# Optimization experiments

Hardware: AMD Instinct MI355X
Metric: run time of the kernel (lower is better)

Reference implementation:

```python
import jax, jax.numpy as jnp
import numpy as np
from jax.scipy.special import logsumexp

C = 1024   # num HMM states
H = 256    # hidden_dim
V = 10000  # vocab size
B = 16     # batch
N = 256    # sequence length
EPS = 1e-5


def _layernorm(x, g, b):
    mu = x.mean(-1, keepdims=True)
    var = ((x - mu) ** 2).mean(-1, keepdims=True)
    return g * (x - mu) * jax.lax.rsqrt(var + EPS) + b


def _residual(x, W1, b1, W2, b2, g, beta):
    # ResidualLayer: ln(relu(lin2(relu(lin1(x)))) + relu(lin1(x))), dropout=0
    h = jax.nn.relu(x @ W1.T + b1)
    return _layernorm(jax.nn.relu(h @ W2.T + b2) + h, g, beta)


def setup_inputs() -> dict:
    key = jax.random.key(0)
    ks = iter(jax.random.split(key, 40))
    def nrm(shape, scale):
        return jax.random.normal(next(ks), shape, dtype=jnp.float32) * scale
    w = 1.0 / np.sqrt(H)
    inp = {}
    # embeddings (torch.randn)
    inp['start_emb'] = nrm((C, H), 1.0)
    inp['state_emb'] = nrm((C, H), 1.0)
    inp['pre_emb'] = nrm((C, H), 1.0)
    # start_mlp: ResidualLayer(H,H) + Linear(H,1)
    for p, out_dim in (('s', 1), ('t', C), ('e', V)):
        inp[p + '_W1'] = nrm((H, H), w)
        inp[p + '_b1'] = jnp.zeros((H,), jnp.float32)
        inp[p + '_W2'] = nrm((H, H), w)
        inp[p + '_b2'] = jnp.zeros((H,), jnp.float32)
        inp[p + '_g'] = jnp.ones((H,), jnp.float32)
        inp[p + '_beta'] = jnp.zeros((H,), jnp.float32)
        inp[p + '_Wo'] = nrm((out_dim, H), w)
        inp[p + '_bo'] = jnp.zeros((out_dim,), jnp.float32)
    inp['text'] = jax.random.randint(next(ks), (B, N), 0, V)
    return inp


def reference(start_emb, state_emb, pre_emb,
              s_W1, s_b1, s_W2, s_b2, s_g, s_beta, s_Wo, s_bo,
              t_W1, t_b1, t_W2, t_b2, t_g, t_beta, t_Wo, t_bo,
              e_W1, e_b1, e_W2, e_b2, e_g, e_beta, e_Wo, e_bo,
              text):
    # start: (C,) log init distribution
    start = jax.nn.log_softmax(
        (_residual(start_emb, s_W1, s_b1, s_W2, s_b2, s_g, s_beta) @ s_Wo.T + s_bo).squeeze(-1))
    # transition[i, j] = log p(z_t = j | z_{t-1} = i), shape (C, C)
    transition = jax.nn.log_softmax(
        _residual(state_emb, t_W1, t_b1, t_W2, t_b2, t_g, t_beta) @ t_Wo.T + t_bo, axis=-1)
    # emission[c, v] = log p(x = v | z = c), shape (C, V)
    emission = jax.nn.log_softmax(
        _residual(pre_emb, e_W1, e_b1, e_W2, e_b2, e_g, e_beta) @ e_Wo.T + e_bo, axis=-1)

    emit = emission.T[text]              # (B, N, C): log p(x_t | z_t = c)
    alpha0 = start[None, :] + emit[:, 0]  # (B, C)

    def step(alpha, e_t):
        # log-semiring matmul: alpha_next[b,j] = lse_i(alpha[b,i] + T[i,j]) + emit
        a = logsumexp(alpha[:, :, None] + transition[None], axis=1) + e_t
        return a, None

    alphaT, _ = jax.lax.scan(step, alpha0, jnp.swapaxes(emit[:, 1:], 0, 1))
    return logsumexp(alphaT, axis=-1).sum()
```

## Files before the change

kernel.cpp:

```cpp
#include <hip/hip_runtime.h>
#include <hip/hip_bf16.h>

typedef __attribute__((ext_vector_type(8))) short short8;
typedef __attribute__((ext_vector_type(4))) float f32x4;
typedef unsigned short ushort;
typedef unsigned long long u64;
typedef unsigned int u32;

#define AL(p) __hip_atomic_load((p), __ATOMIC_RELAXED, __HIP_MEMORY_SCOPE_AGENT)
#define AS(p,v) __hip_atomic_store((p), (v), __ATOMIC_RELAXED, __HIP_MEMORY_SCOPE_AGENT)

__device__ inline ushort f2bf(float x) {
  __hip_bfloat16 h = __float2bfloat16(x);
  return *reinterpret_cast<ushort*>(&h);
}
__device__ inline float bfhi2f(u32 lo) {
  union { u32 u; float f; } c; c.u = lo & 0xFFFF0000u; return c.f;
}
__device__ inline float bflo2f(u32 lo) {
  union { u32 u; float f; } c; c.u = lo << 16; return c.f;
}
__device__ inline u32 pk2(float a, float b) {
  return (u32)f2bf(__expf(a)) | ((u32)f2bf(__expf(b)) << 16);
}

__global__ void cast2_kernel(const float* __restrict__ a, ushort* __restrict__ oa, int na,
                             const float* __restrict__ b, ushort* __restrict__ ob, int nb) {
  int i = blockIdx.x * blockDim.x + threadIdx.x;
  int st = gridDim.x * blockDim.x;
  for (; i < na + nb; i += st) {
    if (i < na) oa[i] = f2bf(a[i]);
    else        ob[i - na] = f2bf(b[i - na]);
  }
}

__global__ __launch_bounds__(256) void mlp3_kernel(
    const float* X0, const float* W10, const float* b10, const float* W20, const float* b20,
    const float* g0, const float* be0, float* of0, ushort* ob0,
    const float* X1, const float* W11, const float* b11, const float* W21, const float* b21,
    const float* g1, const float* be1, float* of1, ushort* ob1,
    const float* X2, const float* W12, const float* b12, const float* W22, const float* b22,
    const float* g2, const float* be2, float* of2, ushort* ob2)
{
  const float *X, *W1, *b1, *W2, *b2, *g, *beta; float* of32; ushort* obf;
  int y = blockIdx.y;
  if (y == 0)      { X=X0; W1=W10; b1=b10; W2=W20; b2=b20; g=g0; beta=be0; of32=of0; obf=ob0; }
  else if (y == 1) { X=X1; W1=W11; b1=b11; W2=W21; b2=b21; g=g1; beta=be1; of32=of1; obf=ob1; }
  else             { X=X2; W1=W12; b1=b12; W2=W22; b2=b22; g=g2; beta=be2; of32=of2; obf=ob2; }

  __shared__ float Xs[16 * 260];
  __shared__ float H1s[16 * 260];
  __shared__ float mu_s[16], rs_s[16];
  int tid = threadIdx.x;
  int r0 = blockIdx.x * 16;
  for (int q = 0; q < 16; ++q) Xs[q * 260 + tid] = X[(r0 + q) * 256 + tid];
  __syncthreads();
  int r = tid & 15, jg = tid >> 4;
  for (int jj = 0; jj < 16; ++jj) {
    int j = jg * 16 + jj;
    const float4* wrow = (const float4*)(W1 + j * 256);
    const float4* xrow = (const float4*)(Xs + r * 260);
    float acc = 0.f;
#pragma unroll 8
    for (int kq = 0; kq < 64; ++kq) {
      float4 w = wrow[kq], x = xrow[kq];
      acc += w.x * x.x + w.y * x.y + w.z * x.z + w.w * x.w;
    }
    acc += b1[j];
    H1s[r * 260 + j] = acc > 0.f ? acc : 0.f;
  }
  __syncthreads();
  for (int jj = 0; jj < 16; ++jj) {
    int j = jg * 16 + jj;
    const float4* wrow = (const float4*)(W2 + j * 256);
    const float4* hrow = (const float4*)(H1s + r * 260);
    float acc = 0.f;
#pragma unroll 8
    for (int kq = 0; kq < 64; ++kq) {
      float4 w = wrow[kq], x = hrow[kq];
      acc += w.x * x.x + w.y * x.y + w.z * x.z + w.w * x.w;
    }
    acc += b2[j];
    float v = (acc > 0.f ? acc : 0.f) + H1s[r * 260 + j];
    Xs[r * 260 + j] = v;
  }
  __syncthreads();
  if (tid < 16) {
    float s = 0.f, s2 = 0.f;
    for (int k = 0; k < 256; ++k) { float x = Xs[tid * 260 + k]; s += x; s2 += x * x; }
    float mu = s * (1.0f / 256.0f);
    float var = s2 * (1.0f / 256.0f) - mu * mu;
    mu_s[tid] = mu; rs_s[tid] = rsqrtf(var + 1e-5f);
  }
  __syncthreads();
  for (int q = 0; q < 16; ++q) {
    float x = (Xs[q * 260 + tid] - mu_s[q]) * rs_s[q] * g[tid] + beta[tid];
    if (of32) of32[(r0 + q) * 256 + tid] = x;
    if (obf)  obf[(r0 + q) * 256 + tid] = f2bf(x);
  }
}

__global__ __launch_bounds__(1024) void shead_kernel(
    const float* __restrict__ h, const float* __restrict__ Wo, const float* __restrict__ bo,
    float* __restrict__ start)
{
  __shared__ float red[16];
  __shared__ float lse_s;
  int tid = threadIdx.x;
  const float4* wr = (const float4*)Wo;
  const float4* hr = (const float4*)(h + tid * 256);
  float acc = 0.f;
  for (int kq = 0; kq < 64; ++kq) {
    float4 w = wr[kq], x = hr[kq];
    acc += w.x * x.x + w.y * x.y + w.z * x.z + w.w * x.w;
  }
  acc += bo[0];
  float s = __expf(acc);
  for (int m = 1; m < 64; m <<= 1) s += __shfl_xor(s, m);
  if ((tid & 63) == 0) red[tid >> 6] = s;
  __syncthreads();
  if (tid == 0) {
    float t = 0.f;
    for (int w = 0; w < 16; ++w) t += red[w];
    lse_s = logf(t);
  }
  __syncthreads();
  start[tid] = acc - lse_s;
}

__global__ __launch_bounds__(256) void gemm_kernel(
    const ushort* __restrict__ A, const ushort* __restrict__ Bw,
    int mode, int Nvalid,
    const float* __restrict__ bias,
    float* __restrict__ out, float* __restrict__ esum, const int* __restrict__ text)
{
  __shared__ ushort As[64 * 264];
  __shared__ ushort Bs[32 * 264];
  int tid = threadIdx.x;
  int m0 = blockIdx.x * 64, n0 = blockIdx.y * 32;
#pragma unroll
  for (int q = 0; q < 8; ++q) {
    int idx = q * 256 + tid;
    int row = idx >> 5, c8 = idx & 31;
    *(short8*)(As + row * 264 + c8 * 8) = *(const short8*)(A + (m0 + row) * 256 + c8 * 8);
  }
#pragma unroll
  for (int q = 0; q < 4; ++q) {
    int idx = q * 256 + tid;
    int row = idx >> 5, c8 = idx & 31;
    int grow = n0 + row;
    short8 val = {0, 0, 0, 0, 0, 0, 0, 0};
    if (mode == 2) {
      int v = text[(grow & 15) * 256 + (grow >> 4)];
      val = *(const short8*)(Bw + v * 256 + c8 * 8);
    } else if (grow < Nvalid) {
      val = *(const short8*)(Bw + grow * 256 + c8 * 8);
    }
    *(short8*)(Bs + row * 264 + c8 * 8) = val;
  }
  __syncthreads();
  int lane = tid & 63, wave = tid >> 6;
  int r16 = lane & 15, quad = lane >> 4;
  f32x4 acc0 = {0.f, 0.f, 0.f, 0.f}, acc1 = {0.f, 0.f, 0.f, 0.f};
#pragma unroll
  for (int kb = 0; kb < 8; ++kb) {
    short8 a  = *(const short8*)(As + (wave * 16 + r16) * 264 + kb * 32 + quad * 8);
    short8 b0 = *(const short8*)(Bs + r16 * 264 + kb * 32 + quad * 8);
    short8 b1 = *(const short8*)(Bs + (16 + r16) * 264 + kb * 32 + quad * 8);
    acc0 = __builtin_amdgcn_mfma_f32_16x16x32_bf16(a, b0, acc0, 0, 0, 0);
    acc1 = __builtin_amdgcn_mfma_f32_16x16x32_bf16(a, b1, acc1, 0, 0, 0);
  }
  if (mode == 0) {
#pragma unroll
    for (int rr = 0; rr < 4; ++rr) {
      int row = m0 + wave * 16 + quad * 4 + rr;
      int c0 = n0 + r16, c1 = n0 + 16 + r16;
      out[row * 1024 + c0] = acc0[rr] + bias[c0];
      out[row * 1024 + c1] = acc1[rr] + bias[c1];
    }
  } else if (mode == 1) {
    float sums[4];
#pragma unroll
    for (int rr = 0; rr < 4; ++rr) {
      int c0 = n0 + r16, c1 = n0 + 16 + r16;
      float p0 = (c0 < Nvalid) ? __expf(acc0[rr] + bias[c0]) : 0.f;
      float p1 = (c1 < Nvalid) ? __expf(acc1[rr] + bias[c1]) : 0.f;
      float s = p0 + p1;
      s += __shfl_xor(s, 1); s += __shfl_xor(s, 2);
      s += __shfl_xor(s, 4); s += __shfl_xor(s, 8);
      sums[rr] = s;
    }
    if (r16 == 0) {
#pragma unroll
      for (int rr = 0; rr < 4; ++rr)
        atomicAdd(esum + m0 + wave * 16 + quad * 4 + rr, sums[rr]);
    }
  } else {
    int c0 = m0 + wave * 16 + quad * 4;
    int tb0 = n0 + r16, tb1 = n0 + 16 + r16;
    int v0 = text[(tb0 & 15) * 256 + (tb0 >> 4)];
    int v1 = text[(tb1 & 15) * 256 + (tb1 >> 4)];
    float l0 = logf(esum[c0]), l1 = logf(esum[c0 + 1]);
    float l2 = logf(esum[c0 + 2]), l3 = logf(esum[c0 + 3]);
    float4 o0, o1;
    o0.x = acc0[0] + bias[v0] - l0; o0.y = acc0[1] + bias[v0] - l1;
    o0.z = acc0[2] + bias[v0] - l2; o0.w = acc0[3] + bias[v0] - l3;
    o1.x = acc1[0] + bias[v1] - l0; o1.y = acc1[1] + bias[v1] - l1;
    o1.z = acc1[2] + bias[v1] - l2; o1.w = acc1[3] + bias[v1] - l3;
    *(float4*)(out + tb0 * 1024 + c0) = o0;
    *(float4*)(out + tb1 * 1024 + c0) = o1;
  }
}

__global__ __launch_bounds__(256) void trans_kernel(
    const float* __restrict__ logits, ushort* __restrict__ texp_frag)
{
  __shared__ float red[4];
  __shared__ float lse_s;
  int i = blockIdx.x, tid = threadIdx.x;
  float x[4];
  float s = 0.f;
#pragma unroll
  for (int q = 0; q < 4; ++q) { x[q] = logits[i * 1024 + q * 256 + tid]; s += __expf(x[q]); }
  for (int m = 1; m < 64; m <<= 1) s += __shfl_xor(s, m);
  if ((tid & 63) == 0) red[tid >> 6] = s;
  __syncthreads();
  if (tid == 0) lse_s = logf(red[0] + red[1] + red[2] + red[3]);
  __syncthreads();
  float lse = lse_s;
  int kblk = i >> 5, quad = (i >> 3) & 3, idx = i & 7;
#pragma unroll
  for (int q = 0; q < 4; ++q) {
    int j = q * 256 + tid;
    int pos = (((j >> 4) * 32 + kblk) * 64 + quad * 16 + (j & 15)) * 8 + idx;
    texp_frag[pos] = f2bf(__expf(x[q] - lse));
  }
}

__global__ __launch_bounds__(256, 1) void scan_kernel(
    const ushort* __restrict__ texp_frag,
    const float* __restrict__ emitg,
    const float* __restrict__ start_v,
    u64* __restrict__ abuf,
    float* __restrict__ out)
{
  __shared__ ushort Ts[4 * 2048 * 8];
  __shared__ __align__(16) char Asb[2][4 * 2080];
  __shared__ float redw[4][4], reds[4][4];

  int tid = threadIdx.x, lane = tid & 63, wave = tid >> 6;
  int r16 = lane & 15, quad = lane >> 4;
  int p = blockIdx.x, bg = p & 3, cb = p >> 2;
  int b0 = bg * 4;

  short8* Ts8 = (short8*)Ts;
  const short8* tfp = (const short8*)texp_frag + (size_t)cb * 8192;
  for (int i = 0; i < 32; ++i) Ts8[i * 256 + tid] = tfp[i * 256 + tid];

  const short8* tsp = Ts8 + wave * 2048;
  int colw = cb * 64 + wave * 16 + r16;
  int abase = (r16 & 3) * 2080 + quad * 16;

  float m_r[4], Bs[4];
#pragma unroll
  for (int i = 0; i < 4; ++i) {
    m_r[i] = start_v[0] + emitg[(size_t)(b0 + i) * 1024];
    Bs[i] = m_r[i];
  }
  {
    int c0 = 2 * tid, c2 = 2 * tid + 512;
    char* ab = Asb[1];
#pragma unroll
    for (int r = 0; r < 4; ++r) {
      const float* eb = emitg + (size_t)(b0 + r) * 1024;
      float v0 = start_v[c0] + eb[c0],     v1 = start_v[c0 + 1] + eb[c0 + 1];
      float v2 = start_v[c2] + eb[c2],     v3 = start_v[c2 + 1] + eb[c2 + 1];
      *(u32*)(ab + r * 2080 + 4 * tid)        = pk2(v0 - m_r[r], v1 - m_r[r]);
      *(u32*)(ab + r * 2080 + 1024 + 4 * tid) = pk2(v2 - m_r[r], v3 - m_r[r]);
    }
  }
  __syncthreads();

  for (int t = 1; t < 256; ++t) {
    float e0 = 0.f, e1 = 0.f, e2 = 0.f, e3 = 0.f;
    if (quad == 0) {
      const float* ep = emitg + (size_t)(t * 16 + b0) * 1024 + colw;
      e0 = ep[0]; e1 = ep[1024]; e2 = ep[2048]; e3 = ep[3072];
    }

    const char* ab = Asb[t & 1];
    f32x4 a0 = {0.f,0.f,0.f,0.f}, a1 = {0.f,0.f,0.f,0.f};
    f32x4 a2 = {0.f,0.f,0.f,0.f}, a3 = {0.f,0.f,0.f,0.f};
#pragma unroll
    for (int kb = 0; kb < 32; kb += 4) {
      short8 f0 = *(const short8*)(ab + abase + kb * 64);
      short8 f1 = *(const short8*)(ab + abase + kb * 64 + 64);
      short8 f2 = *(const short8*)(ab + abase + kb * 64 + 128);
      short8 f3 = *(const short8*)(ab + abase + kb * 64 + 192);
      a0 = __builtin_amdgcn_mfma_f32_16x16x32_bf16(f0, tsp[(kb + 0) * 64 + lane], a0, 0, 0, 0);
      a1 = __builtin_amdgcn_mfma_f32_16x16x32_bf16(f1, tsp[(kb + 1) * 64 + lane], a1, 0, 0, 0);
      a2 = __builtin_amdgcn_mfma_f32_16x16x32_bf16(f2, tsp[(kb + 2) * 64 + lane], a2, 0, 0, 0);
      a3 = __builtin_amdgcn_mfma_f32_16x16x32_bf16(f3, tsp[(kb + 3) * 64 + lane], a3, 0, 0, 0);
    }
    f32x4 acc = (a0 + a1) + (a2 + a3);

    if (quad == 0) {
      float d0 = __logf(acc[0]) + e0;
      float d1 = __logf(acc[1]) + e1;
      float d2 = __logf(acc[2]) + e2;
      float d3 = __logf(acc[3]) + e3;
      u64 tag = ((u64)(u32)t) << 32;
      u64* ob = abuf + (t & 1) * 8192 + bg * 2048 + colw;
      AS(ob,        tag | (u64)((u32)f2bf(d0) | ((u32)f2bf(d1) << 16)));
      AS(ob + 1024, tag | (u64)((u32)f2bf(d2) | ((u32)f2bf(d3) << 16)));
    }

    if (t < 255) {
      u64 x0, x1, x2, x3, x4, x5, x6, x7, n0, n1;
      {
        const u64* buf = abuf + (t & 1) * 8192 + bg * 2048;
        int oa = 2 * tid, oc = 2 * tid + 512;
        u32 want = (u32)t;
        bool first = true;
        for (;;) {
          if (!first) __builtin_amdgcn_s_sleep(1);
          first = false;
          x0 = AL(buf + oa);        x1 = AL(buf + oa + 1);
          x2 = AL(buf + oc);        x3 = AL(buf + oc + 1);
          x4 = AL(buf + 1024 + oa); x5 = AL(buf + 1024 + oa + 1);
          x6 = AL(buf + 1024 + oc); x7 = AL(buf + 1024 + oc + 1);
          n0 = AL(buf);             n1 = AL(buf + 1024);
          u32 bad = ((u32)(x0 >> 32) ^ want) | ((u32)(x1 >> 32) ^ want) |
                    ((u32)(x2 >> 32) ^ want) | ((u32)(x3 >> 32) ^ want) |
                    ((u32)(x4 >> 32) ^ want) | ((u32)(x5 >> 32) ^ want) |
                    ((u32)(x6 >> 32) ^ want) | ((u32)(x7 >> 32) ^ want) |
                    ((u32)(n0 >> 32) ^ want) | ((u32)(n1 >> 32) ^ want);
          if (bad == 0) break;
        }
      }
      m_r[0] = bflo2f((u32)n0); m_r[1] = bfhi2f((u32)n0);
      m_r[2] = bflo2f((u32)n1); m_r[3] = bfhi2f((u32)n1);
      Bs[0] += m_r[0]; Bs[1] += m_r[1]; Bs[2] += m_r[2]; Bs[3] += m_r[3];

      char* aw = Asb[(t + 1) & 1];
      u32 l0 = (u32)x0, l1 = (u32)x1, l2 = (u32)x2, l3 = (u32)x3;
      u32 l4 = (u32)x4, l5 = (u32)x5, l6 = (u32)x6, l7 = (u32)x7;
      *(u32*)(aw + 4 * tid)                = pk2(bflo2f(l0) - m_r[0], bflo2f(l1) - m_r[0]);
      *(u32*)(aw + 1024 + 4 * tid)         = pk2(bflo2f(l2) - m_r[0], bflo2f(l3) - m_r[0]);
      *(u32*)(aw + 2080 + 4 * tid)         = pk2(bfhi2f(l0) - m_r[1], bfhi2f(l1) - m_r[1]);
      *(u32*)(aw + 2080 + 1024 + 4 * tid)  = pk2(bfhi2f(l2) - m_r[1], bfhi2f(l3) - m_r[1]);
      *(u32*)(aw + 4160 + 4 * tid)         = pk2(bflo2f(l4) - m_r[2], bflo2f(l5) - m_r[2]);
      *(u32*)(aw + 4160 + 1024 + 4 * tid)  = pk2(bflo2f(l6) - m_r[2], bflo2f(l7) - m_r[2]);
      *(u32*)(aw + 6240 + 4 * tid)         = pk2(bfhi2f(l4) - m_r[3], bfhi2f(l5) - m_r[3]);
      *(u32*)(aw + 6240 + 1024 + 4 * tid)  = pk2(bfhi2f(l6) - m_r[3], bfhi2f(l7) - m_r[3]);
      __syncthreads();
    }
  }

  if (cb == 0) {
    const u64* fb = abuf + 8192 + bg * 2048;
    int oa = 2 * tid, oc = 2 * tid + 512;
    u64 x0, x1, x2, x3, x4, x5, x6, x7;
    {
      bool first = true;
      for (;;) {
        if (!first) __builtin_amdgcn_s_sleep(1);
        first = false;
        x0 = AL(fb + oa);        x1 = AL(fb + oa + 1);
        x2 = AL(fb + oc);        x3 = AL(fb + oc + 1);
        x4 = AL(fb + 1024 + oa); x5 = AL(fb + 1024 + oa + 1);
        x6 = AL(fb + 1024 + oc); x7 = AL(fb + 1024 + oc + 1);
        u32 bad = ((u32)(x0 >> 32) ^ 255u) | ((u32)(x1 >> 32) ^ 255u) |
                  ((u32)(x2 >> 32) ^ 255u) | ((u32)(x3 >> 32) ^ 255u) |
                  ((u32)(x4 >> 32) ^ 255u) | ((u32)(x5 >> 32) ^ 255u) |
                  ((u32)(x6 >> 32) ^ 255u) | ((u32)(x7 >> 32) ^ 255u);
        if (bad == 0) break;
      }
    }
    float bv[4][4];
    bv[0][0] = bflo2f((u32)x0); bv[0][1] = bflo2f((u32)x1); bv[0][2] = bflo2f((u32)x2); bv[0][3] = bflo2f((u32)x3);
    bv[1][0] = bfhi2f((u32)x0); bv[1][1] = bfhi2f((u32)x1); bv[1][2] = bfhi2f((u32)x2); bv[1][3] = bfhi2f((u32)x3);
    bv[2][0] = bflo2f((u32)x4); bv[2][1] = bflo2f((u32)x5); bv[2][2] = bflo2f((u32)x6); bv[2][3] = bflo2f((u32)x7);
    bv[3][0] = bfhi2f((u32)x4); bv[3][1] = bfhi2f((u32)x5); bv[3][2] = bfhi2f((u32)x6); bv[3][3] = bfhi2f((u32)x7);
    float M[4], S[4];
#pragma unroll
    for (int i = 0; i < 4; ++i)
      M[i] = fmaxf(fmaxf(bv[i][0], bv[i][1]), fmaxf(bv[i][2], bv[i][3]));
    for (int off = 1; off < 64; off <<= 1) {
#pragma unroll
      for (int i = 0; i < 4; ++i) M[i] = fmaxf(M[i], __shfl_xor(M[i], off));
    }
    if (lane == 0) { redw[wave][0]=M[0]; redw[wave][1]=M[1]; redw[wave][2]=M[2]; redw[wave][3]=M[3]; }
    __syncthreads();
#pragma unroll
    for (int i = 0; i < 4; ++i)
      M[i] = fmaxf(fmaxf(redw[0][i], redw[1][i]), fmaxf(redw[2][i], redw[3][i]));
#pragma unroll
    for (int i = 0; i < 4; ++i)
      S[i] = __expf(bv[i][0] - M[i]) + __expf(bv[i][1] - M[i]) +
             __expf(bv[i][2] - M[i]) + __expf(bv[i][3] - M[i]);
    for (int off = 1; off < 64; off <<= 1) {
#pragma unroll
      for (int i = 0; i < 4; ++i) S[i] += __shfl_xor(S[i], off);
    }
    if (lane == 0) { reds[wave][0]=S[0]; reds[wave][1]=S[1]; reds[wave][2]=S[2]; reds[wave][3]=S[3]; }
    __syncthreads();
    if (tid == 0) {
      float tot = 0.f;
#pragma unroll
      for (int i = 0; i < 4; ++i) {
        float Sg = reds[0][i] + reds[1][i] + reds[2][i] + reds[3][i];
        tot += Bs[i] + M[i] + logf(Sg);
      }
      atomicAdd(out, tot);
    }
  }
}

extern "C" void kernel_launch(void* const* d_in, const int* in_sizes, int n_in,
                              void* d_out, int out_size, void* d_ws, size_t ws_size,
                              hipStream_t stream)
{
  (void)in_sizes; (void)n_in; (void)out_size; (void)ws_size;
  const float* start_emb = (const float*)d_in[0];
  const float* state_emb = (const float*)d_in[1];
  const float* pre_emb   = (const float*)d_in[2];
  const float* s_W1 = (const float*)d_in[3];  const float* s_b1 = (const float*)d_in[4];
  const float* s_W2 = (const float*)d_in[5];  const float* s_b2 = (const float*)d_in[6];
  const float* s_g  = (const float*)d_in[7];  const float* s_be = (const float*)d_in[8];
  const float* s_Wo = (const float*)d_in[9];  const float* s_bo = (const float*)d_in[10];
  const float* t_W1 = (const float*)d_in[11]; const float* t_b1 = (const float*)d_in[12];
  const float* t_W2 = (const float*)d_in[13]; const float* t_b2 = (const float*)d_in[14];
  const float* t_g  = (const float*)d_in[15]; const float* t_be = (const float*)d_in[16];
  const float* t_Wo = (const float*)d_in[17]; const float* t_bo = (const float*)d_in[18];
  const float* e_W1 = (const float*)d_in[19]; const float* e_b1 = (const float*)d_in[20];
  const float* e_W2 = (const float*)d_in[21]; const float* e_b2 = (const float*)d_in[22];
  const float* e_g  = (const float*)d_in[23]; const float* e_be = (const float*)d_in[24];
  const float* e_Wo = (const float*)d_in[25]; const float* e_bo = (const float*)d_in[26];
  const int*   text = (const int*)d_in[27];
  float* out = (float*)d_out;

  char* ws = (char*)d_ws;
  size_t off = 0;
  auto alloc = [&](size_t bytes) -> char* {
    char* p = ws + off;
    off = (off + bytes + 255) & ~(size_t)255;
    return p;
  };
  float* esum       = (float*)alloc(1024 * 4);
  u64*   abuf       = (u64*)alloc(2 * 8192 * 8);
  float* start_v    = (float*)alloc(1024 * 4);
  float* h_s        = (float*)alloc(1024 * 256 * 4);
  ushort* h_t_bf    = (ushort*)alloc(1024 * 256 * 2);
  ushort* h_e_bf    = (ushort*)alloc(1024 * 256 * 2);
  ushort* tWo_bf    = (ushort*)alloc(1024 * 256 * 2);
  ushort* eWo_bf    = (ushort*)alloc(10000 * 256 * 2);
  float* tlogits    = (float*)alloc(1024 * 1024 * 4);
  ushort* texp_frag = (ushort*)alloc(1024 * 1024 * 2);
  float* emitg      = (float*)alloc(4096 * 1024 * 4);

  hipMemsetAsync(ws, 0, 4096 + 2 * 8192 * 8, stream);
  hipMemsetAsync(d_out, 0, 4, stream);

  cast2_kernel<<<768, 256, 0, stream>>>(t_Wo, tWo_bf, 1024 * 256, e_Wo, eWo_bf, 10000 * 256);

  mlp3_kernel<<<dim3(64, 3), 256, 0, stream>>>(
      start_emb, s_W1, s_b1, s_W2, s_b2, s_g, s_be, h_s, nullptr,
      state_emb, t_W1, t_b1, t_W2, t_b2, t_g, t_be, nullptr, h_t_bf,
      pre_emb,  e_W1, e_b1, e_W2, e_b2, e_g, e_be, nullptr, h_e_bf);

  shead_kernel<<<1, 1024, 0, stream>>>(h_s, s_Wo, s_bo, start_v);

  gemm_kernel<<<dim3(16, 32),  256, 0, stream>>>(h_t_bf, tWo_bf, 0, 1024,  t_bo, tlogits, nullptr, nullptr);
  trans_kernel<<<1024, 256, 0, stream>>>(tlogits, texp_frag);
  gemm_kernel<<<dim3(16, 313), 256, 0, stream>>>(h_e_bf, eWo_bf, 1, 10000, e_bo, nullptr, esum, nullptr);
  gemm_kernel<<<dim3(16, 128), 256, 0, stream>>>(h_e_bf, eWo_bf, 2, 4096,  e_bo, emitg, esum, text);

  scan_kernel<<<64, 256, 0, stream>>>(texp_frag, emitg, start_v, abuf, out);
}
```

Before: 977.1 us.

## Run scan in linear probability space and keep transition fragments in registers

The forward scan now exchanges probabilities instead of log values. Each step multiplies the matmul result by exp(emission), and the next step rescales by the reciprocal of a reference entry rather than calling exp and log on every element. This removes per-element transcendental work from the serial critical path, and the final reduction drops its max pass. The transition B-fragments are loaded once into 32 short8 registers per thread instead of LDS, which removes the LDS reads in the MFMA loop. The trade-offs are high register pressure, and a risk of bf16 underflow or overflow, since the scaling uses column 0 rather than the maximum.

```diff
diff --git a/kernel.cpp b/kernel.cpp
--- a/kernel.cpp
+++ b/kernel.cpp
@@ -22,6 +22,9 @@
 }
 __device__ inline u32 pk2(float a, float b) {
   return (u32)f2bf(__expf(a)) | ((u32)f2bf(__expf(b)) << 16);
+}
+__device__ inline u32 pk2m(float a, float b) {
+  return (u32)f2bf(a) | ((u32)f2bf(b) << 16);
 }
 
 __global__ void cast2_kernel(const float* __restrict__ a, ushort* __restrict__ oa, int na,
@@ -244,20 +247,19 @@
     u64* __restrict__ abuf,
     float* __restrict__ out)
 {
-  __shared__ ushort Ts[4 * 2048 * 8];
   __shared__ __align__(16) char Asb[2][4 * 2080];
-  __shared__ float redw[4][4], reds[4][4];
+  __shared__ float reds[4][4];
 
   int tid = threadIdx.x, lane = tid & 63, wave = tid >> 6;
   int r16 = lane & 15, quad = lane >> 4;
   int p = blockIdx.x, bg = p & 3, cb = p >> 2;
   int b0 = bg * 4;
 
-  short8* Ts8 = (short8*)Ts;
-  const short8* tfp = (const short8*)texp_frag + (size_t)cb * 8192;
-  for (int i = 0; i < 32; ++i) Ts8[i * 256 + tid] = tfp[i * 256 + tid];
-
-  const short8* tsp = Ts8 + wave * 2048;
+  const short8* tg = (const short8*)texp_frag + (size_t)cb * 8192 + wave * 2048;
+  short8 treg[32];
+#pragma unroll
+  for (int k = 0; k < 32; ++k) treg[k] = tg[k * 64 + lane];
+
   int colw = cb * 64 + wave * 16 + r16;
   int abase = (r16 & 3) * 2080 + quad * 16;
 
@@ -282,10 +284,11 @@
   __syncthreads();
 
   for (int t = 1; t < 256; ++t) {
-    float e0 = 0.f, e1 = 0.f, e2 = 0.f, e3 = 0.f;
+    float E0 = 0.f, E1 = 0.f, E2 = 0.f, E3 = 0.f;
     if (quad == 0) {
       const float* ep = emitg + (size_t)(t * 16 + b0) * 1024 + colw;
-      e0 = ep[0]; e1 = ep[1024]; e2 = ep[2048]; e3 = ep[3072];
+      E0 = __expf(ep[0]); E1 = __expf(ep[1024]);
+      E2 = __expf(ep[2048]); E3 = __expf(ep[3072]);
     }
 
     const char* ab = Asb[t & 1];
@@ -297,22 +300,20 @@
       short8 f1 = *(const short8*)(ab + abase + kb * 64 + 64);
       short8 f2 = *(const short8*)(ab + abase + kb * 64 + 128);
       short8 f3 = *(const short8*)(ab + abase + kb * 64 + 192);
-      a0 = __builtin_amdgcn_mfma_f32_16x16x32_bf16(f0, tsp[(kb + 0) * 64 + lane], a0, 0, 0, 0);
-      a1 = __builtin_amdgcn_mfma_f32_16x16x32_bf16(f1, tsp[(kb + 1) * 64 + lane], a1, 0, 0, 0);
-      a2 = __builtin_amdgcn_mfma_f32_16x16x32_bf16(f2, tsp[(kb + 2) * 64 + lane], a2, 0, 0, 0);
-      a3 = __builtin_amdgcn_mfma_f32_16x16x32_bf16(f3, tsp[(kb + 3) * 64 + lane], a3, 0, 0, 0);
+      a0 = __builtin_amdgcn_mfma_f32_16x16x32_bf16(f0, treg[kb + 0], a0, 0, 0, 0);
+      a1 = __builtin_amdgcn_mfma_f32_16x16x32_bf16(f1, treg[kb + 1], a1, 0, 0, 0);
+      a2 = __builtin_amdgcn_mfma_f32_16x16x32_bf16(f2, treg[kb + 2], a2, 0, 0, 0);
+      a3 = __builtin_amdgcn_mfma_f32_16x16x32_bf16(f3, treg[kb + 3], a3, 0, 0, 0);
     }
     f32x4 acc = (a0 + a1) + (a2 + a3);
 
     if (quad == 0) {
-      float d0 = __logf(acc[0]) + e0;
-      float d1 = __logf(acc[1]) + e1;
-      float d2 = __logf(acc[2]) + e2;
-      float d3 = __logf(acc[3]) + e3;
+      float P0 = acc[0] * E0, P1 = acc[1] * E1;
+      float P2 = acc[2] * E2, P3 = acc[3] * E3;
       u64 tag = ((u64)(u32)t) << 32;
       u64* ob = abuf + (t & 1) * 8192 + bg * 2048 + colw;
-      AS(ob,        tag | (u64)((u32)f2bf(d0) | ((u32)f2bf(d1) << 16)));
-      AS(ob + 1024, tag | (u64)((u32)f2bf(d2) | ((u32)f2bf(d3) << 16)));
+      AS(ob,        tag | (u64)pk2m(P0, P1));
+      AS(ob + 1024, tag | (u64)pk2m(P2, P3));
     }
 
     if (t < 255) {
@@ -340,19 +341,24 @@
       }
       m_r[0] = bflo2f((u32)n0); m_r[1] = bfhi2f((u32)n0);
       m_r[2] = bflo2f((u32)n1); m_r[3] = bfhi2f((u32)n1);
-      Bs[0] += m_r[0]; Bs[1] += m_r[1]; Bs[2] += m_r[2]; Bs[3] += m_r[3];
+      float r0 = __builtin_amdgcn_rcpf(m_r[0]);
+      float r1 = __builtin_amdgcn_rcpf(m_r[1]);
+      float r2 = __builtin_amdgcn_rcpf(m_r[2]);
+      float r3 = __builtin_amdgcn_rcpf(m_r[3]);
+      Bs[0] += __logf(m_r[0]); Bs[1] += __logf(m_r[1]);
+      Bs[2] += __logf(m_r[2]); Bs[3] += __logf(m_r[3]);
 
       char* aw = Asb[(t + 1) & 1];
       u32 l0 = (u32)x0, l1 = (u32)x1, l2 = (u32)x2, l3 = (u32)x3;
       u32 l4 = (u32)x4, l5 = (u32)x5, l6 = (u32)x6, l7 = (u32)x7;
-      *(u32*)(aw + 4 * tid)                = pk2(bflo2f(l0) - m_r[0], bflo2f(l1) - m_r[0]);
-      *(u32*)(aw + 1024 + 4 * tid)         = pk2(bflo2f(l2) - m_r[0], bflo2f(l3) - m_r[0]);
-      *(u32*)(aw + 2080 + 4 * tid)         = pk2(bfhi2f(l0) - m_r[1], bfhi2f(l1) - m_r[1]);
-      *(u32*)(aw + 2080 + 1024 + 4 * tid)  = pk2(bfhi2f(l2) - m_r[1], bfhi2f(l3) - m_r[1]);
-      *(u32*)(aw + 4160 + 4 * tid)         = pk2(bflo2f(l4) - m_r[2], bflo2f(l5) - m_r[2]);
-      *(u32*)(aw + 4160 + 1024 + 4 * tid)  = pk2(bflo2f(l6) - m_r[2], bflo2f(l7) - m_r[2]);
-      *(u32*)(aw + 6240 + 4 * tid)         = pk2(bfhi2f(l4) - m_r[3], bfhi2f(l5) - m_r[3]);
-      *(u32*)(aw + 6240 + 1024 + 4 * tid)  = pk2(bfhi2f(l6) - m_r[3], bfhi2f(l7) - m_r[3]);
+      *(u32*)(aw + 4 * tid)                = pk2m(bflo2f(l0) * r0, bflo2f(l1) * r0);
+      *(u32*)(aw + 1024 + 4 * tid)         = pk2m(bflo2f(l2) * r0, bflo2f(l3) * r0);
+      *(u32*)(aw + 2080 + 4 * tid)         = pk2m(bfhi2f(l0) * r1, bfhi2f(l1) * r1);
+      *(u32*)(aw + 2080 + 1024 + 4 * tid)  = pk2m(bfhi2f(l2) * r1, bfhi2f(l3) * r1);
+      *(u32*)(aw + 4160 + 4 * tid)         = pk2m(bflo2f(l4) * r2, bflo2f(l5) * r2);
+      *(u32*)(aw + 4160 + 1024 + 4 * tid)  = pk2m(bflo2f(l6) * r2, bflo2f(l7) * r2);
+      *(u32*)(aw + 6240 + 4 * tid)         = pk2m(bfhi2f(l4) * r3, bfhi2f(l5) * r3);
+      *(u32*)(aw + 6240 + 1024 + 4 * tid)  = pk2m(bfhi2f(l6) * r3, bfhi2f(l7) * r3);
       __syncthreads();
     }
   }
@@ -377,28 +383,11 @@
         if (bad == 0) break;
       }
     }
-    float bv[4][4];
-    bv[0][0] = bflo2f((u32)x0); bv[0][1] = bflo2f((u32)x1); bv[0][2] = bflo2f((u32)x2); bv[0][3] = bflo2f((u32)x3);
-    bv[1][0] = bfhi2f((u32)x0); bv[1][1] = bfhi2f((u32)x1); bv[1][2] = bfhi2f((u32)x2); bv[1][3] = bfhi2f((u32)x3);
-    bv[2][0] = bflo2f((u32)x4); bv[2][1] = bflo2f((u32)x5); bv[2][2] = bflo2f((u32)x6); bv[2][3] = bflo2f((u32)x7);
-    bv[3][0] = bfhi2f((u32)x4); bv[3][1] = bfhi2f((u32)x5); bv[3][2] = bfhi2f((u32)x6); bv[3][3] = bfhi2f((u32)x7);
-    float M[4], S[4];
-#pragma unroll
-    for (int i = 0; i < 4; ++i)
-      M[i] = fmaxf(fmaxf(bv[i][0], bv[i][1]), fmaxf(bv[i][2], bv[i][3]));
-    for (int off = 1; off < 64; off <<= 1) {
-#pragma unroll
-      for (int i = 0; i < 4; ++i) M[i] = fmaxf(M[i], __shfl_xor(M[i], off));
-    }
-    if (lane == 0) { redw[wave][0]=M[0]; redw[wave][1]=M[1]; redw[wave][2]=M[2]; redw[wave][3]=M[3]; }
-    __syncthreads();
-#pragma unroll
-    for (int i = 0; i < 4; ++i)
-      M[i] = fmaxf(fmaxf(redw[0][i], redw[1][i]), fmaxf(redw[2][i], redw[3][i]));
-#pragma unroll
-    for (int i = 0; i < 4; ++i)
-      S[i] = __expf(bv[i][0] - M[i]) + __expf(bv[i][1] - M[i]) +
-             __expf(bv[i][2] - M[i]) + __expf(bv[i][3] - M[i]);
+    float S[4];
+    S[0] = bflo2f((u32)x0) + bflo2f((u32)x1) + bflo2f((u32)x2) + bflo2f((u32)x3);
+    S[1] = bfhi2f((u32)x0) + bfhi2f((u32)x1) + bfhi2f((u32)x2) + bfhi2f((u32)x3);
+    S[2] = bflo2f((u32)x4) + bflo2f((u32)x5) + bflo2f((u32)x6) + bflo2f((u32)x7);
+    S[3] = bfhi2f((u32)x4) + bfhi2f((u32)x5) + bfhi2f((u32)x6) + bfhi2f((u32)x7);
     for (int off = 1; off < 64; off <<= 1) {
 #pragma unroll
       for (int i = 0; i < 4; ++i) S[i] += __shfl_xor(S[i], off);
@@ -410,7 +399,7 @@
 #pragma unroll
       for (int i = 0; i < 4; ++i) {
         float Sg = reds[0][i] + reds[1][i] + reds[2][i] + reds[3][i];
-        tot += Bs[i] + M[i] + logf(Sg);
+        tot += Bs[i] + logf(Sg);
       }
       atomicAdd(out, tot);
     }
```

Result: slower. 1.022 ms (+4.5%).
